# Kernel optimization log

Hardware: AMD Instinct MI355X
Metric: run time of the kernel (lower is better)

## Reference

```python
import jax, jax.numpy as jnp
import numpy as np

INPUT_SIZE = 512   # num_embeddings == RNN input feature dim
SEQ = INPUT_SIZE // 4   # 128, embedding dim == RNN seq_len
HID = 12
OUT = 3
B = 2048


def setup_inputs() -> dict:
    key = jax.random.key(0)
    ks = jax.random.split(key, 12)
    s = 0.1
    x = jax.random.randint(ks[0], (B, INPUT_SIZE), 0, INPUT_SIZE)
    emb = jax.random.normal(ks[1], (INPUT_SIZE, SEQ), dtype=jnp.float32) * s
    w_ih_f = jax.random.normal(ks[2], (HID, INPUT_SIZE), dtype=jnp.float32) * s
    w_hh_f = jax.random.normal(ks[3], (HID, HID), dtype=jnp.float32) * s
    b_ih_f = jax.random.normal(ks[4], (HID,), dtype=jnp.float32) * s
    b_hh_f = jax.random.normal(ks[5], (HID,), dtype=jnp.float32) * s
    w_ih_r = jax.random.normal(ks[6], (HID, INPUT_SIZE), dtype=jnp.float32) * s
    w_hh_r = jax.random.normal(ks[7], (HID, HID), dtype=jnp.float32) * s
    b_ih_r = jax.random.normal(ks[8], (HID,), dtype=jnp.float32) * s
    b_hh_r = jax.random.normal(ks[9], (HID,), dtype=jnp.float32) * s
    fc_w = jax.random.normal(ks[10], (OUT, 2 * HID), dtype=jnp.float32) * s
    fc_b = jax.random.normal(ks[11], (OUT,), dtype=jnp.float32) * s
    return {"x": x, "emb": emb,
            "w_ih_f": w_ih_f, "w_hh_f": w_hh_f, "b_ih_f": b_ih_f, "b_hh_f": b_hh_f,
            "w_ih_r": w_ih_r, "w_hh_r": w_hh_r, "b_ih_r": b_ih_r, "b_hh_r": b_hh_r,
            "fc_w": fc_w, "fc_b": fc_b}


def reference(x, emb, w_ih_f, w_hh_f, b_ih_f, b_hh_f,
              w_ih_r, w_hh_r, b_ih_r, b_hh_r, fc_w, fc_b):
    # embedding lookup: (B, INPUT_SIZE) -> (B, INPUT_SIZE, SEQ)
    e = emb[x]
    # view(-1, input_size, seq) is a no-op on this contiguous shape; swapaxes(1,2)
    xs = jnp.swapaxes(e, 1, 2)  # (B, SEQ, INPUT_SIZE): seq_len=SEQ, feat=INPUT_SIZE

    # forward-direction tanh RNN: precompute input projections, scan the recurrence
    pre = jnp.einsum('bsi,hi->sbh', xs, w_ih_f) + b_ih_f  # (SEQ, B, HID)

    def step(h, p):
        h = jnp.tanh(p + h @ w_hh_f.T + b_hh_f)
        return h, None

    h0 = jnp.zeros((xs.shape[0], HID), dtype=xs.dtype)
    h_fwd, _ = jax.lax.scan(step, h0, pre)  # final forward hidden (B, HID)

    # reverse-direction output at the LAST timestep = one step from zero hidden
    # on x_{T-1} (only out[:, -1, :] is consumed by the module)
    h_bwd = jnp.tanh(xs[:, -1, :] @ w_ih_r.T + b_ih_r + b_hh_r)  # (B, HID)

    out_last = jnp.concatenate([h_fwd, h_bwd], axis=-1)  # (B, 2*HID)
    return out_last @ fc_w.T + fc_b  # (B, OUT)
```

## Files before the change

kernel.cpp:

```cpp
#include <hip/hip_runtime.h>
#include <hip/hip_bf16.h>

#define B_N     2048
#define IN_N    512
#define SEQ_N   128
#define HID_N   12
#define HP_N    16
#define OUT_N   3

typedef __attribute__((ext_vector_type(8))) short short8;
typedef __attribute__((ext_vector_type(4))) float f32x4;
typedef unsigned int uint;
typedef unsigned short ushort;

__device__ __forceinline__ float fast_tanh(float x) {
    float e = __builtin_amdgcn_exp2f(x * 2.8853900817779268f);
    return 1.0f - 2.0f * __builtin_amdgcn_rcpf(e + 1.0f);
}

__device__ __forceinline__ ushort f2bf(float f) {
    uint u = __float_as_uint(f);
    u += 0x7fffu + ((u >> 16) & 1u);
    return (ushort)(u >> 16);
}

__device__ __forceinline__ float bf2f(ushort s) {
    return __uint_as_float(((uint)s) << 16);
}

__global__ __launch_bounds__(256) void k_prep(
    const float* __restrict__ emb, const float* __restrict__ w_ih_f,
    const float* __restrict__ w_ih_r,
    ushort* __restrict__ embB, ushort* __restrict__ wP)
{
    int tid = blockIdx.x * 256 + threadIdx.x;
    float4 e = ((const float4*)emb)[tid];
    uint2 o;
    o.x = (uint)f2bf(e.x) | ((uint)f2bf(e.y) << 16);
    o.y = (uint)f2bf(e.z) | ((uint)f2bf(e.w) << 16);
    ((uint2*)embB)[tid] = o;

    int j   = tid & 7;
    int l   = (tid >> 3) & 63;
    int src = (tid >> 9) & 1;
    int cks = tid >> 10;
    int h   = l & 15;
    int i   = (cks >> 2) * 128 + (cks & 3) * 32 + (l >> 4) * 8 + j;
    const float* wsrc = src ? w_ih_r : w_ih_f;
    wP[(((size_t)cks * 2 + src) * 64 + l) * 8 + j] =
        (h < HID_N) ? f2bf(wsrc[h * IN_N + i]) : (ushort)0;
}

__global__ __launch_bounds__(256, 2) void k_pre(
    const int* __restrict__ x, const ushort* __restrict__ embB,
    const ushort* __restrict__ wP,
    const float* __restrict__ b_ih_r, const float* __restrict__ b_hh_r,
    ushort* __restrict__ preB, float* __restrict__ rev)
{
    __shared__ __align__(16) ushort As[128 * 128];
    __shared__ __align__(16) ushort wPs[16384];

    const int t      = threadIdx.x;
    const int l      = t & 63;
    const int w      = t >> 6;
    const int lane16 = l & 15;
    const int quad   = l >> 4;
    const int il     = w * 32 + quad * 8;
    const int wg     = w * 4 + quad;
    const int l7     = lane16 & 7;
    const int so     = lane16 * 8;
    const int b0     = blockIdx.x * 4;

    {
        const uint4* s4 = (const uint4*)wP;
        uint4*       d4 = (uint4*)wPs;
        #pragma unroll
        for (int i = 0; i < 8; ++i) d4[t + i * 256] = s4[t + i * 256];
    }

    f32x4 a0_0={0.f,0.f,0.f,0.f}, a0_1={0.f,0.f,0.f,0.f}, a0_2={0.f,0.f,0.f,0.f}, a0_3={0.f,0.f,0.f,0.f};
    f32x4 a1_0={0.f,0.f,0.f,0.f}, a1_1={0.f,0.f,0.f,0.f}, a1_2={0.f,0.f,0.f,0.f}, a1_3={0.f,0.f,0.f,0.f};
    f32x4 aR_0={0.f,0.f,0.f,0.f}, aR_1={0.f,0.f,0.f,0.f}, aR_2={0.f,0.f,0.f,0.f}, aR_3={0.f,0.f,0.f,0.f};

    uint RA[8][4], RB[8][4];
    int4 IA0, IA1, IB0, IB1;

#define IDXLD(Ilo, Ihi, bq2, c2) do { \
    const int* xq_ = x + (size_t)(b0 + (bq2)) * IN_N + (c2) * 128 + il; \
    Ilo = *(const int4*)xq_;  Ihi = *(const int4*)(xq_ + 4); \
} while (0)

#define GFETCH(Rb, Ilo, Ihi) do { uint4 v_; \
    v_ = *(const uint4*)(embB + (size_t)(Ilo).x * SEQ_N + so); Rb[0][0]=v_.x; Rb[0][1]=v_.y; Rb[0][2]=v_.z; Rb[0][3]=v_.w; \
    v_ = *(const uint4*)(embB + (size_t)(Ilo).y * SEQ_N + so); Rb[1][0]=v_.x; Rb[1][1]=v_.y; Rb[1][2]=v_.z; Rb[1][3]=v_.w; \
    v_ = *(const uint4*)(embB + (size_t)(Ilo).z * SEQ_N + so); Rb[2][0]=v_.x; Rb[2][1]=v_.y; Rb[2][2]=v_.z; Rb[2][3]=v_.w; \
    v_ = *(const uint4*)(embB + (size_t)(Ilo).w * SEQ_N + so); Rb[3][0]=v_.x; Rb[3][1]=v_.y; Rb[3][2]=v_.z; Rb[3][3]=v_.w; \
    v_ = *(const uint4*)(embB + (size_t)(Ihi).x * SEQ_N + so); Rb[4][0]=v_.x; Rb[4][1]=v_.y; Rb[4][2]=v_.z; Rb[4][3]=v_.w; \
    v_ = *(const uint4*)(embB + (size_t)(Ihi).y * SEQ_N + so); Rb[5][0]=v_.x; Rb[5][1]=v_.y; Rb[5][2]=v_.z; Rb[5][3]=v_.w; \
    v_ = *(const uint4*)(embB + (size_t)(Ihi).z * SEQ_N + so); Rb[6][0]=v_.x; Rb[6][1]=v_.y; Rb[6][2]=v_.z; Rb[6][3]=v_.w; \
    v_ = *(const uint4*)(embB + (size_t)(Ihi).w * SEQ_N + so); Rb[7][0]=v_.x; Rb[7][1]=v_.y; Rb[7][2]=v_.z; Rb[7][3]=v_.w; \
} while (0)

#define PACKR(Rb) do { \
    _Pragma("unroll") \
    for (int pp = 0; pp < 8; ++pp) { \
        const uint sel_ = (pp & 1) ? 0x07060302u : 0x05040100u; \
        const int pv_ = pp >> 1; \
        uint u0_ = __builtin_amdgcn_perm(Rb[1][pv_], Rb[0][pv_], sel_); \
        uint u1_ = __builtin_amdgcn_perm(Rb[3][pv_], Rb[2][pv_], sel_); \
        uint u2_ = __builtin_amdgcn_perm(Rb[5][pv_], Rb[4][pv_], sel_); \
        uint u3_ = __builtin_amdgcn_perm(Rb[7][pv_], Rb[6][pv_], sel_); \
        const int s_    = lane16 * 8 + pp; \
        const int slot_ = wg ^ pp ^ l7; \
        *(uint4*)&As[(size_t)s_ * 128 + (size_t)slot_ * 8] = make_uint4(u0_, u1_, u2_, u3_); \
    } \
} while (0)

#define MMA(A0, A1, AR) do { \
    _Pragma("unroll") \
    for (int tt = 0; tt < 2; ++tt) { \
        const int row_ = (w * 2 + tt) * 16 + lane16; \
        const int fr_  = (row_ & 7) ^ ((row_ >> 3) & 7); \
        _Pragma("unroll") \
        for (int ks = 0; ks < 4; ++ks) { \
            const int slot_ = (ks * 4 + quad) ^ fr_; \
            short8 af_ = *(const short8*)&As[(size_t)row_ * 128 + (size_t)slot_ * 8]; \
            if (tt == 0) { A0 = __builtin_amdgcn_mfma_f32_16x16x32_bf16(af_, bfr[ks], A0, 0, 0, 0); } \
            else { A1 = __builtin_amdgcn_mfma_f32_16x16x32_bf16(af_, bfr[ks], A1, 0, 0, 0); \
                   AR = __builtin_amdgcn_mfma_f32_16x16x32_bf16(af_, bfrR[ks], AR, 0, 0, 0); } \
        } \
    } \
} while (0)

    IDXLD(IA0, IA1, 0, 0);
    IDXLD(IB0, IB1, 1, 0);
    GFETCH(RA, IA0, IA1);
    GFETCH(RB, IB0, IB1);
    IDXLD(IA0, IA1, 2, 0);

    for (int c = 0; c < 4; ++c) {
        short8 bfr[4], bfrR[4];
        #pragma unroll
        for (int bq = 0; bq < 4; ++bq) {
            if (bq & 1) PACKR(RB); else PACKR(RA);

            if (!(c == 3 && bq >= 2)) {
                if (bq & 1) GFETCH(RB, IB0, IB1); else GFETCH(RA, IA0, IA1);
            }
            if (!(c == 3 && bq >= 1)) {
                if      (bq == 0) IDXLD(IB0, IB1, 3, c);
                else if (bq == 1) IDXLD(IA0, IA1, 0, c + 1);
                else if (bq == 2) IDXLD(IB0, IB1, 1, c + 1);
                else              IDXLD(IA0, IA1, 2, c + 1);
            }

            asm volatile("s_waitcnt lgkmcnt(0)" ::: "memory");
            __builtin_amdgcn_s_barrier();
            __builtin_amdgcn_sched_barrier(0);

            if (bq == 0) {
                #pragma unroll
                for (int ks = 0; ks < 4; ++ks) {
                    const ushort* wp = wPs + (size_t)((c * 4 + ks) * 128 + l) * 8;
                    bfr[ks]  = *(const short8*)wp;
                    bfrR[ks] = *(const short8*)(wp + 512);
                }
            }

            if      (bq == 0) MMA(a0_0, a1_0, aR_0);
            else if (bq == 1) MMA(a0_1, a1_1, aR_1);
            else if (bq == 2) MMA(a0_2, a1_2, aR_2);
            else              MMA(a0_3, a1_3, aR_3);

            asm volatile("" ::: "memory");
            __builtin_amdgcn_s_barrier();
            __builtin_amdgcn_sched_barrier(0);
        }
    }

#define EPI(bq, A0, A1, AR) do { \
    const int bcur_ = b0 + (bq); \
    _Pragma("unroll") \
    for (int r = 0; r < 4; ++r) { \
        const int s0_ = (w * 2 + 0) * 16 + quad * 4 + r; \
        preB[((size_t)bcur_ * SEQ_N + s0_) * HP_N + lane16] = f2bf(A0[r]); \
        const int s1_ = (w * 2 + 1) * 16 + quad * 4 + r; \
        preB[((size_t)bcur_ * SEQ_N + s1_) * HP_N + lane16] = f2bf(A1[r]); \
    } \
    if (w == 3 && quad == 3) \
        rev[bcur_ * HP_N + lane16] = fast_tanh(AR[3] + b_ih_r[lane16] + b_hh_r[lane16]); \
} while (0)

    if (lane16 < HID_N) {
        EPI(0, a0_0, a1_0, aR_0);
        EPI(1, a0_1, a1_1, aR_1);
        EPI(2, a0_2, a1_2, aR_2);
        EPI(3, a0_3, a1_3, aR_3);
    }
#undef IDXLD
#undef GFETCH
#undef PACKR
#undef MMA
#undef EPI
}

__global__ __launch_bounds__(256) void k_rnn(
    const ushort* __restrict__ preB, const float* __restrict__ rev,
    const float* __restrict__ w_hh_f,
    const float* __restrict__ b_ih_f, const float* __restrict__ b_hh_f,
    const float* __restrict__ fc_w, const float* __restrict__ fc_b,
    float* __restrict__ out)
{
    __shared__ float ho[16][40];

    const int tid = threadIdx.x;
    const int l   = tid & 63;
    const int j   = l & 15;
    const int jj  = (j < 12) ? j : 0;
    const int gid = tid >> 4;
    const int b   = blockIdx.x * 16 + gid;
    const int baseaddr = (l & 48) << 2;

    const float4* wr = (const float4*)(w_hh_f + jj * 12);
    float4 w0 = wr[0], w1 = wr[1], w2 = wr[2];
    float W[12] = {w0.x, w0.y, w0.z, w0.w, w1.x, w1.y, w1.z, w1.w,
                   w2.x, w2.y, w2.z, w2.w};
    const float bias = b_ih_f[jj] + b_hh_f[jj];

    const ushort* pb = preB + (size_t)b * SEQ_N * HP_N + j;
    ushort pq[8];
    #pragma unroll
    for (int k = 0; k < 8; ++k) pq[k] = pb[k * HP_N];

    float h = 0.f;
    for (int s8 = 0; s8 < 16; ++s8) {
        #pragma unroll
        for (int k = 0; k < 8; ++k) {
            int s = s8 * 8 + k;
            float p = bf2f(pq[k]) + bias;
            pq[k] = pb[((s + 8) & 127) * HP_N];
            int hb = __float_as_int(h);
            float hk[12];
            #pragma unroll
            for (int kk = 0; kk < 12; ++kk)
                hk[kk] = __int_as_float(__builtin_amdgcn_ds_bpermute(baseaddr + 4 * kk, hb));
            float c0 = p, c1 = 0.f, c2 = 0.f;
            #pragma unroll
            for (int u = 0; u < 4; ++u) {
                c0 = __builtin_fmaf(W[u],     hk[u],     c0);
                c1 = __builtin_fmaf(W[4 + u], hk[4 + u], c1);
                c2 = __builtin_fmaf(W[8 + u], hk[8 + u], c2);
            }
            h = fast_tanh(c0 + c1 + c2);
        }
    }

    ho[gid][j]      = h;
    ho[gid][20 + j] = rev[b * HP_N + j];
    if (j < OUT_N) {
        const float* fw = fc_w + j * 24;
        float o = fc_b[j];
        #pragma unroll
        for (int k = 0; k < 12; ++k)
            o += fw[k] * ho[gid][k] + fw[12 + k] * ho[gid][20 + k];
        out[b * OUT_N + j] = o;
    }
}

extern "C" void kernel_launch(void* const* d_in, const int* in_sizes, int n_in,
                              void* d_out, int out_size, void* d_ws, size_t ws_size,
                              hipStream_t stream) {
    const int*   x      = (const int*)  d_in[0];
    const float* emb    = (const float*)d_in[1];
    const float* w_ih_f = (const float*)d_in[2];
    const float* w_hh_f = (const float*)d_in[3];
    const float* b_ih_f = (const float*)d_in[4];
    const float* b_hh_f = (const float*)d_in[5];
    const float* w_ih_r = (const float*)d_in[6];
    const float* b_ih_r = (const float*)d_in[8];
    const float* b_hh_r = (const float*)d_in[9];
    const float* fc_w   = (const float*)d_in[10];
    const float* fc_b   = (const float*)d_in[11];
    float* out = (float*)d_out;

    ushort* preB = (ushort*)d_ws;
    float*  rev  = (float*)((char*)d_ws + 8388608);
    ushort* embB = (ushort*)((char*)d_ws + 8519680);
    ushort* wP   = (ushort*)((char*)d_ws + 8650752);

    k_prep<<<64,    256, 0, stream>>>(emb, w_ih_f, w_ih_r, embB, wP);
    k_pre <<<B_N/4, 256, 0, stream>>>(x, embB, wP, b_ih_r, b_hh_r, preB, rev);
    k_rnn <<<B_N/16,256, 0, stream>>>(preB, rev, w_hh_f, b_ih_f, b_hh_f, fc_w, fc_b, out);
}
```

Before: 117.8 us.

## Run RNN recurrence with per-step fp16 MFMA instead of bpermute broadcasts

Each recurrence step now does the hidden-state matvec with one 16x16x16 fp16 MFMA per wave, covering 16 batch rows, instead of 12 ds_bpermute broadcasts plus scalar FMAs. The hidden state stays in MFMA operand layout, so it feeds the next step without any cross-lane shuffles. The tanh scale factor is folded into the weights and biases, and each block now handles 64 batch rows, giving 32 blocks. In exchange, the hidden state and weights drop to fp16 precision, and far fewer blocks are launched.

```diff
diff --git a/kernel.cpp b/kernel.cpp
--- a/kernel.cpp
+++ b/kernel.cpp
@@ -10,11 +10,17 @@
 
 typedef __attribute__((ext_vector_type(8))) short short8;
 typedef __attribute__((ext_vector_type(4))) float f32x4;
+typedef __attribute__((ext_vector_type(4))) _Float16 f16x4;
 typedef unsigned int uint;
 typedef unsigned short ushort;
 
 __device__ __forceinline__ float fast_tanh(float x) {
     float e = __builtin_amdgcn_exp2f(x * 2.8853900817779268f);
+    return 1.0f - 2.0f * __builtin_amdgcn_rcpf(e + 1.0f);
+}
+
+__device__ __forceinline__ float tanh_ps(float x) {
+    float e = __builtin_amdgcn_exp2f(x);
     return 1.0f - 2.0f * __builtin_amdgcn_rcpf(e + 1.0f);
 }
 
@@ -211,59 +217,94 @@
     const float* __restrict__ fc_w, const float* __restrict__ fc_b,
     float* __restrict__ out)
 {
-    __shared__ float ho[16][40];
-
-    const int tid = threadIdx.x;
-    const int l   = tid & 63;
-    const int j   = l & 15;
-    const int jj  = (j < 12) ? j : 0;
-    const int gid = tid >> 4;
-    const int b   = blockIdx.x * 16 + gid;
-    const int baseaddr = (l & 48) << 2;
-
-    const float4* wr = (const float4*)(w_hh_f + jj * 12);
-    float4 w0 = wr[0], w1 = wr[1], w2 = wr[2];
-    float W[12] = {w0.x, w0.y, w0.z, w0.w, w1.x, w1.y, w1.z, w1.w,
-                   w2.x, w2.y, w2.z, w2.w};
-    const float bias = b_ih_f[jj] + b_hh_f[jj];
-
-    const ushort* pb = preB + (size_t)b * SEQ_N * HP_N + j;
-    ushort pq[8];
+    __shared__ float ho[64][16];
+
+    const int t      = threadIdx.x;
+    const int l      = t & 63;
+    const int wv     = t >> 6;
+    const int lane16 = l & 15;
+    const int quad   = l >> 4;
+    const int bloc   = wv * 16 + lane16;
+    const int b      = blockIdx.x * 64 + bloc;
+
+    const float SC = 2.8853900817779268f;
+
+    f16x4 aW;
+    {
+        float w0_=0.f, w1_=0.f, w2_=0.f, w3_=0.f;
+        if (lane16 < HID_N && quad < 3) {
+            const float* wr = w_hh_f + lane16 * 12 + quad * 4;
+            w0_ = wr[0]; w1_ = wr[1]; w2_ = wr[2]; w3_ = wr[3];
+        }
+        aW[0] = (_Float16)(SC * w0_);
+        aW[1] = (_Float16)(SC * w1_);
+        aW[2] = (_Float16)(SC * w2_);
+        aW[3] = (_Float16)(SC * w3_);
+    }
+
+    float bias0=0.f, bias1=0.f, bias2=0.f, bias3=0.f;
+    if (quad < 3) {
+        const int h = quad * 4;
+        bias0 = SC * (b_ih_f[h]     + b_hh_f[h]);
+        bias1 = SC * (b_ih_f[h + 1] + b_hh_f[h + 1]);
+        bias2 = SC * (b_ih_f[h + 2] + b_hh_f[h + 2]);
+        bias3 = SC * (b_ih_f[h + 3] + b_hh_f[h + 3]);
+    }
+
+    const ushort* pb = preB + (size_t)b * SEQ_N * HP_N + quad * 4;
+    uint2 pq[16];
     #pragma unroll
-    for (int k = 0; k < 8; ++k) pq[k] = pb[k * HP_N];
-
-    float h = 0.f;
-    for (int s8 = 0; s8 < 16; ++s8) {
-        #pragma unroll
-        for (int k = 0; k < 8; ++k) {
-            int s = s8 * 8 + k;
-            float p = bf2f(pq[k]) + bias;
-            pq[k] = pb[((s + 8) & 127) * HP_N];
-            int hb = __float_as_int(h);
-            float hk[12];
+    for (int k = 0; k < 16; ++k) pq[k] = *(const uint2*)(pb + k * HP_N);
+
+    f16x4 hB = {(_Float16)0.f, (_Float16)0.f, (_Float16)0.f, (_Float16)0.f};
+    float t0 = 0.f, t1 = 0.f, t2 = 0.f, t3 = 0.f;
+
+    for (int s16 = 0; s16 < 8; ++s16) {
+        #pragma unroll
+        for (int k = 0; k < 16; ++k) {
+            const int s = s16 * 16 + k;
+            uint2 pv = pq[k];
+            float c0 = __builtin_fmaf(bf2f((ushort)(pv.x & 0xffffu)), SC, bias0);
+            float c1 = __builtin_fmaf(bf2f((ushort)(pv.x >> 16)),     SC, bias1);
+            float c2 = __builtin_fmaf(bf2f((ushort)(pv.y & 0xffffu)), SC, bias2);
+            float c3 = __builtin_fmaf(bf2f((ushort)(pv.y >> 16)),     SC, bias3);
+            if (quad == 3) { c0 = 0.f; c1 = 0.f; c2 = 0.f; c3 = 0.f; }
+            pq[k] = *(const uint2*)(pb + ((s + 16) & 127) * HP_N);
+            f32x4 cc = {c0, c1, c2, c3};
+            f32x4 d = __builtin_amdgcn_mfma_f32_16x16x16f16(aW, hB, cc, 0, 0, 0);
+            t0 = tanh_ps(d[0]);
+            t1 = tanh_ps(d[1]);
+            t2 = tanh_ps(d[2]);
+            t3 = tanh_ps(d[3]);
+            f16x4 nh;
+            nh[0] = (_Float16)t0;
+            nh[1] = (_Float16)t1;
+            nh[2] = (_Float16)t2;
+            nh[3] = (_Float16)t3;
+            hB = nh;
+        }
+    }
+
+    *(float4*)&ho[bloc][quad * 4] = make_float4(t0, t1, t2, t3);
+    if (quad == 0) {
+        float4 h0 = *(const float4*)&ho[bloc][0];
+        float4 h1 = *(const float4*)&ho[bloc][4];
+        float4 h2 = *(const float4*)&ho[bloc][8];
+        float hv[12] = {h0.x,h0.y,h0.z,h0.w, h1.x,h1.y,h1.z,h1.w,
+                        h2.x,h2.y,h2.z,h2.w};
+        const float* rv = rev + b * HP_N;
+        float rvv[12];
+        #pragma unroll
+        for (int k2 = 0; k2 < 12; ++k2) rvv[k2] = rv[k2];
+        #pragma unroll
+        for (int o = 0; o < OUT_N; ++o) {
+            const float* fw = fc_w + o * 24;
+            float acc = fc_b[o];
             #pragma unroll
-            for (int kk = 0; kk < 12; ++kk)
-                hk[kk] = __int_as_float(__builtin_amdgcn_ds_bpermute(baseaddr + 4 * kk, hb));
-            float c0 = p, c1 = 0.f, c2 = 0.f;
-            #pragma unroll
-            for (int u = 0; u < 4; ++u) {
-                c0 = __builtin_fmaf(W[u],     hk[u],     c0);
-                c1 = __builtin_fmaf(W[4 + u], hk[4 + u], c1);
-                c2 = __builtin_fmaf(W[8 + u], hk[8 + u], c2);
-            }
-            h = fast_tanh(c0 + c1 + c2);
+            for (int k2 = 0; k2 < 12; ++k2)
+                acc += fw[k2] * hv[k2] + fw[12 + k2] * rvv[k2];
+            out[b * OUT_N + o] = acc;
         }
-    }
-
-    ho[gid][j]      = h;
-    ho[gid][20 + j] = rev[b * HP_N + j];
-    if (j < OUT_N) {
-        const float* fw = fc_w + j * 24;
-        float o = fc_b[j];
-        #pragma unroll
-        for (int k = 0; k < 12; ++k)
-            o += fw[k] * ho[gid][k] + fw[12 + k] * ho[gid][20 + k];
-        out[b * OUT_N + j] = o;
     }
 }
 
@@ -290,5 +331,5 @@
 
     k_prep<<<64,    256, 0, stream>>>(emb, w_ih_f, w_ih_r, embB, wP);
     k_pre <<<B_N/4, 256, 0, stream>>>(x, embB, wP, b_ih_r, b_hh_r, preB, rev);
-    k_rnn <<<B_N/16,256, 0, stream>>>(preB, rev, w_hh_f, b_ih_f, b_hh_f, fc_w, fc_b, out);
-}
+    k_rnn <<<B_N/64,256, 0, stream>>>(preB, rev, w_hh_f, b_ih_f, b_hh_f, fc_w, fc_b, out);
+}
```

New measurement: 116.2 us. No clear change (-1.4%).
